# Kernel optimization log

Hardware: AMD Instinct MI355X
Metric: run time of the kernel (lower is better)

The kernel has to match this reference:

```python
import jax, jax.numpy as jnp
import numpy as np

B, T, HOR = 4096, 128, 24
EH, DH, A = 64, 64, 32


def setup_inputs() -> dict:
    key = jax.random.key(0)
    ks = jax.random.split(key, 21)
    g = lambda k, shape, s=0.1: (jax.random.normal(k, shape, jnp.float32) * s)
    return {
        "x": jax.random.normal(ks[0], (B, T, 1), jnp.float32),
        # encoder GRUCell (input_size=1)
        "W_ih_e": g(ks[1], (3 * EH, 1)), "W_hh_e": g(ks[2], (3 * EH, EH)),
        "b_ih_e": g(ks[3], (3 * EH,)), "b_hh_e": g(ks[4], (3 * EH,)),
        # encoder input attention
        "W_e": g(ks[5], (A, EH)), "U_e": g(ks[6], (1, A)),
        "b_e": jnp.zeros((1, A), jnp.float32), "v_e": g(ks[7], (A,)),
        # decoder init
        "W_init": g(ks[8], (DH, EH)), "b_init": g(ks[9], (DH,)),
        # decoder GRUCell (input_size=1)
        "W_ih_d": g(ks[10], (3 * DH, 1)), "W_hh_d": g(ks[11], (3 * DH, DH)),
        "b_ih_d": g(ks[12], (3 * DH,)), "b_hh_d": g(ks[13], (3 * DH,)),
        # temporal attention
        "W_d": g(ks[14], (A, DH)), "U_d": g(ks[15], (A, EH)), "v_d": g(ks[16], (A,)),
        # output head
        "W_out": g(ks[17], (1, DH + EH)), "b_out": g(ks[18], (1,)),
        "y0": jnp.zeros((1,), jnp.float32),
    }


def _gru_cell(x, h, W_ih, W_hh, b_ih, b_hh):
    # PyTorch GRUCell semantics
    gi = x @ W_ih.T + b_ih  # (B, 3H)
    gh = h @ W_hh.T + b_hh
    ir, iz, inn = jnp.split(gi, 3, axis=1)
    hr, hz, hn = jnp.split(gh, 3, axis=1)
    r = jax.nn.sigmoid(ir + hr)
    z = jax.nn.sigmoid(iz + hz)
    n = jnp.tanh(inn + r * hn)
    return (1.0 - z) * n + z * h


def reference(x, W_ih_e, W_hh_e, b_ih_e, b_hh_e, W_e, U_e, b_e, v_e,
              W_init, b_init, W_ih_d, W_hh_d, b_ih_d, b_hh_d,
              W_d, U_d, v_d, W_out, b_out, y0):
    bsz = x.shape[0]

    def enc_step(h, x_t):  # x_t: (B, 1)
        h_proj = h @ W_e.T  # (B, A)
        attn = jnp.tanh(h_proj[:, None, :] + x_t[:, :, None] * U_e[None] + b_e[None])  # (B,1,A)
        scores = jnp.sum(attn * v_e, axis=2)  # (B, 1)
        alpha = jax.nn.softmax(scores, axis=1)
        h_new = _gru_cell(alpha * x_t, h, W_ih_e, W_hh_e, b_ih_e, b_hh_e)
        return h_new, h_new

    h0 = jnp.zeros((bsz, EH), x.dtype)
    h_T, Hs = jax.lax.scan(enc_step, h0, jnp.swapaxes(x, 0, 1))  # Hs: (T,B,EH)
    H = jnp.swapaxes(Hs, 0, 1)  # (B, T, EH)

    d0 = h_T @ W_init.T + b_init  # (B, DH)
    H_proj = jnp.einsum('bte,ae->bta', H, U_d)  # hoisted: constant across decoder steps
    dec_in0 = jnp.broadcast_to(y0[None, :], (bsz, 1))

    def dec_step(carry, _):
        d, dec_in = carry
        d = _gru_cell(dec_in, d, W_ih_d, W_hh_d, b_ih_d, b_hh_d)
        d_proj = d @ W_d.T  # (B, A)
        attn = jnp.tanh(d_proj[:, None, :] + H_proj)  # (B, T, A)
        beta = jax.nn.softmax(jnp.sum(attn * v_d, axis=2), axis=1)  # (B, T)
        ctx = jnp.einsum('bt,bte->be', beta, H)  # (B, EH)
        out = jnp.concatenate([d, ctx], axis=1) @ W_out.T + b_out  # (B, 1)
        return (d, out), out[:, 0]

    (_, _), outs = jax.lax.scan(dec_step, (d0, dec_in0), None, length=HOR)
    return outs.T  # (B, horizon)
```

## Files before the change

kernel.cpp:

```cpp
#include <hip/hip_runtime.h>
#include <math.h>

#define BATCH 4096
#define T 128
#define HOR 24

#define LOG2E 1.44269504088896f
#define C2    2.88539008177793f

typedef _Float16 half2_t __attribute__((ext_vector_type(2)));
typedef _Float16 half8   __attribute__((ext_vector_type(8)));
typedef float f2  __attribute__((ext_vector_type(2)));
typedef float f4v __attribute__((ext_vector_type(4)));

__device__ __forceinline__ float fexp2(float x){ return __builtin_amdgcn_exp2f(x); }
__device__ __forceinline__ float frcp(float x){ return __builtin_amdgcn_rcpf(x); }
__device__ __forceinline__ float fsig(float x){ return frcp(1.0f + fexp2(-LOG2E*x)); }
__device__ __forceinline__ float ftanh(float x){ return fmaf(-2.0f, frcp(1.0f + fexp2(C2*x)), 1.0f); }
__device__ __forceinline__ half2_t bch(unsigned u){ return __builtin_bit_cast(half2_t,u); }
__device__ __forceinline__ unsigned pk2(float a,float b){ return __builtin_bit_cast(unsigned, __builtin_amdgcn_cvt_pkrtz(a,b)); }
__device__ __forceinline__ unsigned pk2rne(float a,float b){
  half2_t h; h.x = (_Float16)a; h.y = (_Float16)b;
  return __builtin_bit_cast(unsigned, h);
}
__device__ __forceinline__ float fdot2f(half2_t a, half2_t b, float c){
#if __has_builtin(__builtin_amdgcn_fdot2)
  return __builtin_amdgcn_fdot2(a,b,c,false);
#else
  return fmaf((float)a.x,(float)b.x, fmaf((float)a.y,(float)b.y,c));
#endif
}
__device__ __forceinline__ f2 pkfma(f2 a, f2 b, f2 c){ return __builtin_elementwise_fma(a,b,c); }

template <int CTRL, int RMASK>
__device__ __forceinline__ float dpp_add(float v) {
  int s = __builtin_amdgcn_update_dpp(0, __builtin_bit_cast(int, v), CTRL, RMASK, 0xf, true);
  return v + __builtin_bit_cast(float, s);
}
__device__ __forceinline__ float wavesum_dpp(float v) {
  v = dpp_add<0x111, 0xf>(v);
  v = dpp_add<0x112, 0xf>(v);
  v = dpp_add<0x114, 0xf>(v);
  v = dpp_add<0x118, 0xf>(v);
  v = dpp_add<0x142, 0xa>(v);
  v = dpp_add<0x143, 0xc>(v);
  return v;
}
__device__ __forceinline__ float rdl63(float v){
  return __builtin_bit_cast(float, __builtin_amdgcn_readlane(__builtin_bit_cast(int, v), 63));
}

#define WG_BARRIER_LDS() do {                                   \
    asm volatile("s_waitcnt lgkmcnt(0)" ::: "memory");          \
    __builtin_amdgcn_s_barrier();                               \
  } while (0)

__device__ __forceinline__ void gru_mv(const _Float16* hrow,
    const unsigned* wr_r, const unsigned* wr_z, const unsigned* wr_n,
    float& ar0, float& ar1, float& az0, float& az1, float& an0, float& an1)
{
  const uint4* hq = (const uint4*)hrow;
  #pragma unroll
  for (int q = 0; q < 8; ++q) {
    uint4 hv = hq[q];
    ar0 = fdot2f(bch(hv.x), bch(wr_r[4*q+0]), ar0);
    az0 = fdot2f(bch(hv.x), bch(wr_z[4*q+0]), az0);
    an0 = fdot2f(bch(hv.x), bch(wr_n[4*q+0]), an0);
    ar1 = fdot2f(bch(hv.y), bch(wr_r[4*q+1]), ar1);
    az1 = fdot2f(bch(hv.y), bch(wr_z[4*q+1]), az1);
    an1 = fdot2f(bch(hv.y), bch(wr_n[4*q+1]), an1);
    ar0 = fdot2f(bch(hv.z), bch(wr_r[4*q+2]), ar0);
    az0 = fdot2f(bch(hv.z), bch(wr_z[4*q+2]), az0);
    an0 = fdot2f(bch(hv.z), bch(wr_n[4*q+2]), an0);
    ar1 = fdot2f(bch(hv.w), bch(wr_r[4*q+3]), ar1);
    az1 = fdot2f(bch(hv.w), bch(wr_z[4*q+3]), az1);
    an1 = fdot2f(bch(hv.w), bch(wr_n[4*q+3]), an1);
  }
}

__device__ __forceinline__ float proj_dot(const _Float16* base, const unsigned* udr)
{
  float acc = 0.f;
  const uint4* hb = (const uint4*)base;
  #pragma unroll
  for (int q = 0; q < 4; ++q) {
    uint4 hv = hb[q];
    acc = fdot2f(bch(hv.x), bch(udr[4*q+0]), acc);
    acc = fdot2f(bch(hv.y), bch(udr[4*q+1]), acc);
    acc = fdot2f(bch(hv.z), bch(udr[4*q+2]), acc);
    acc = fdot2f(bch(hv.w), bch(udr[4*q+3]), acc);
  }
  return acc;
}

__device__ __forceinline__ half8 cvt8(f4v a, f4v b){
  half8 h;
  h[0]=(_Float16)a.x; h[1]=(_Float16)a.y; h[2]=(_Float16)a.z; h[3]=(_Float16)a.w;
  h[4]=(_Float16)b.x; h[5]=(_Float16)b.y; h[6]=(_Float16)b.z; h[7]=(_Float16)b.w;
  return h;
}

__device__ __forceinline__ float grp4(float acc, f4v ed,
                                      half2_t ha, half2_t hb,
                                      float v0, float v1, float v2, float v3)
{
  float a0 = fmaf(ed.x, (float)ha.x, 1.0f);
  float a1 = fmaf(ed.y, (float)ha.y, 1.0f);
  float a2 = fmaf(ed.z, (float)hb.x, 1.0f);
  float a3 = fmaf(ed.w, (float)hb.y, 1.0f);
  float d01 = a0 * a1;
  float d23 = a2 * a3;
  float n01 = fmaf(v0, a1, v1 * a0);
  float n23 = fmaf(v2, a3, v3 * a2);
  float nc  = fmaf(n01, d23, n23 * d01);
  return fmaf(nc, frcp(d01 * d23), acc);
}

__global__ __launch_bounds__(256, 1)
void darnn_enc(const float* __restrict__ x,
               const float* __restrict__ W_ih_e, const float* __restrict__ W_hh_e,
               const float* __restrict__ b_ih_e, const float* __restrict__ b_hh_e,
               const float* __restrict__ U_d, const float* __restrict__ W_out,
               unsigned* __restrict__ hpG, float* __restrict__ hTG)
{
  const int tid = threadIdx.x;
  const int w = tid >> 6;
  const int l = tid & 63;
  const int c = l & 15;
  const int q = l >> 4;
  const int e0 = blockIdx.x * 16;
  const int m0 = 16*w + 4*q;

  __shared__ __align__(16) _Float16 He[2][16*72];
  __shared__ __align__(16) unsigned xw[16*65];

  for (int idx = tid; idx < 16*64; idx += 256) {
    int e = idx >> 6, j = idx & 63;
    f2 g = ((const f2*)(x + (size_t)(e0+e)*T))[j];
    xw[e*65 + j] = pk2(g.x, g.y);
  }
  for (int idx = tid; idx < 576; idx += 256) ((unsigned*)He[0])[idx] = 0;

  half8 Ar[2], Az[2], An[2];
  #pragma unroll
  for (int kap = 0; kap < 2; ++kap) {
    const f4v* pr = (const f4v*)(W_hh_e + (size_t)(16*w + c)*64       + 32*kap + 8*q);
    const f4v* pz = (const f4v*)(W_hh_e + (size_t)(64 + 16*w + c)*64  + 32*kap + 8*q);
    const f4v* pn = (const f4v*)(W_hh_e + (size_t)(128 + 16*w + c)*64 + 32*kap + 8*q);
    Ar[kap] = cvt8(pr[0], pr[1]);
    Az[kap] = cvt8(pz[0], pz[1]);
    An[kap] = cvt8(pn[0], pn[1]);
  }
  half8 AX[2] = {{0,0,0,0,0,0,0,0},{0,0,0,0,0,0,0,0}};
  if (w < 2) {
    #pragma unroll
    for (int kap = 0; kap < 2; ++kap) {
      const f4v* p = (const f4v*)(U_d + (size_t)(16*w + c)*64 + 32*kap + 8*q);
      AX[kap] = cvt8(p[0] * C2, p[1] * C2);
    }
  } else if (w == 2 && c == 0) {
    #pragma unroll
    for (int kap = 0; kap < 2; ++kap) {
      const f4v* p = (const f4v*)(W_out + 64 + 32*kap + 8*q);
      AX[kap] = cvt8(p[0], p[1]);
    }
  }
  f4v wih0 = *(const f4v*)(W_ih_e + m0);
  f4v wih1 = *(const f4v*)(W_ih_e + 64 + m0);
  f4v wih2 = *(const f4v*)(W_ih_e + 128 + m0);
  f4v bb0  = *(const f4v*)(b_ih_e + m0)      + *(const f4v*)(b_hh_e + m0);
  f4v bb1  = *(const f4v*)(b_ih_e + 64 + m0) + *(const f4v*)(b_hh_e + 64 + m0);
  f4v bi2  = *(const f4v*)(b_ih_e + 128 + m0);
  f4v bh2  = *(const f4v*)(b_hh_e + 128 + m0);
  f4v hreg = {0,0,0,0};
  const f4v z4 = {0,0,0,0};
  unsigned* hpB = hpG + (size_t)(e0 + c) * 2176;

  __syncthreads();

  #pragma unroll 1
  for (int t = 0; t < T; ++t) {
    const _Float16* Hc = He[t & 1];
    half8 B0 = __builtin_bit_cast(half8, *(const uint4*)(Hc + c*72 + 8*q));
    half8 B1 = __builtin_bit_cast(half8, *(const uint4*)(Hc + c*72 + 32 + 8*q));
    if (t > 0) {
      if (w < 2) {
        f4v cu = __builtin_amdgcn_mfma_f32_16x16x32_f16(AX[0], B0, z4, 0,0,0);
        cu     = __builtin_amdgcn_mfma_f32_16x16x32_f16(AX[1], B1, cu, 0,0,0);
        unsigned* hpE = hpB + (t-1)*17 + 8*w;
        float x0 = fexp2(fminf(cu[0], 15.5f));
        float x1 = fexp2(fminf(cu[1], 15.5f));
        float x2 = fexp2(fminf(cu[2], 15.5f));
        float x3 = fexp2(fminf(cu[3], 15.5f));
        hpE[2*q]   = pk2rne(x0, x1);
        hpE[2*q+1] = pk2rne(x2, x3);
      } else if (w == 2) {
        f4v cw = __builtin_amdgcn_mfma_f32_16x16x32_f16(AX[0], B0, z4, 0,0,0);
        cw     = __builtin_amdgcn_mfma_f32_16x16x32_f16(AX[1], B1, cw, 0,0,0);
        if (q == 0) ((float*)(hpB + (t-1)*17))[16] = cw[0];
      }
    }
    f4v gr = __builtin_amdgcn_mfma_f32_16x16x32_f16(Ar[0], B0, z4, 0,0,0);
    gr     = __builtin_amdgcn_mfma_f32_16x16x32_f16(Ar[1], B1, gr, 0,0,0);
    f4v gz = __builtin_amdgcn_mfma_f32_16x16x32_f16(Az[0], B0, z4, 0,0,0);
    gz     = __builtin_amdgcn_mfma_f32_16x16x32_f16(Az[1], B1, gz, 0,0,0);
    f4v gn = __builtin_amdgcn_mfma_f32_16x16x32_f16(An[0], B0, z4, 0,0,0);
    gn     = __builtin_amdgcn_mfma_f32_16x16x32_f16(An[1], B1, gn, 0,0,0);
    float xc = (float)((const _Float16*)xw)[c*130 + t];
    f4v hn;
    #pragma unroll
    for (int i = 0; i < 4; ++i) {
      float r  = fsig(fmaf(xc, wih0[i], bb0[i]) + gr[i]);
      float zf = fsig(fmaf(xc, wih1[i], bb1[i]) + gz[i]);
      float n  = ftanh(fmaf(xc, wih2[i], bi2[i]) + r*(gn[i] + bh2[i]));
      float h  = fmaf(zf, hreg[i] - n, n);
      hreg[i] = h;
      hn[i] = h;
    }
    uint2 wv; wv.x = pk2(hn[0], hn[1]); wv.y = pk2(hn[2], hn[3]);
    *(uint2*)(He[(t+1)&1] + c*72 + m0) = wv;
    WG_BARRIER_LDS();
  }
  {
    const _Float16* Hc = He[0];
    half8 B0 = __builtin_bit_cast(half8, *(const uint4*)(Hc + c*72 + 8*q));
    half8 B1 = __builtin_bit_cast(half8, *(const uint4*)(Hc + c*72 + 32 + 8*q));
    if (w < 2) {
      f4v cu = __builtin_amdgcn_mfma_f32_16x16x32_f16(AX[0], B0, z4, 0,0,0);
      cu     = __builtin_amdgcn_mfma_f32_16x16x32_f16(AX[1], B1, cu, 0,0,0);
      unsigned* hpE = hpB + 127*17 + 8*w;
      float x0 = fexp2(fminf(cu[0], 15.5f));
      float x1 = fexp2(fminf(cu[1], 15.5f));
      float x2 = fexp2(fminf(cu[2], 15.5f));
      float x3 = fexp2(fminf(cu[3], 15.5f));
      hpE[2*q]   = pk2rne(x0, x1);
      hpE[2*q+1] = pk2rne(x2, x3);
    } else if (w == 2) {
      f4v cw = __builtin_amdgcn_mfma_f32_16x16x32_f16(AX[0], B0, z4, 0,0,0);
      cw     = __builtin_amdgcn_mfma_f32_16x16x32_f16(AX[1], B1, cw, 0,0,0);
      if (q == 0) ((float*)(hpB + 127*17))[16] = cw[0];
    }
  }
  #pragma unroll
  for (int i = 0; i < 4; ++i)
    hTG[(size_t)(e0 + c)*64 + m0 + i] = hreg[i];
}

__global__ __launch_bounds__(128, 2)
void darnn_dec(const float* __restrict__ W_init, const float* __restrict__ b_init,
               const float* __restrict__ W_ih_d, const float* __restrict__ W_hh_d,
               const float* __restrict__ b_ih_d, const float* __restrict__ b_hh_d,
               const float* __restrict__ W_d, const float* __restrict__ v_d,
               const float* __restrict__ W_out, const float* __restrict__ b_out,
               const float* __restrict__ y0,
               const unsigned* __restrict__ hpG, const float* __restrict__ hTG,
               float* __restrict__ out)
{
  const int tid = threadIdx.x;
  const int wid = tid >> 6;
  const int l   = tid & 63;
  const int bA  = 4*blockIdx.x + 2*wid;
  const int bB  = bA + 1;
  const int a    = l & 31;
  const int half = l >> 5;

  __shared__ __align__(16) unsigned char smem[36928];
  unsigned char* wbp = smem + wid*18464;
  unsigned* hpA   = (unsigned*)wbp;
  unsigned* hpB   = (unsigned*)(wbp + 8704);
  _Float16* ringA = (_Float16*)(wbp + 17408);
  _Float16* ringB = (_Float16*)(wbp + 17536);
  float*    dpA   = (float*)(wbp + 17664);
  float*    dpB   = (float*)(wbp + 17792);
  float*    hTA   = (float*)(wbp + 17920);
  float*    hTB   = (float*)(wbp + 18176);

  {
    const uint4* sA = (const uint4*)(hpG + (size_t)bA * 2176);
    const uint4* sB = (const uint4*)(hpG + (size_t)bB * 2176);
    #pragma unroll
    for (int it = 0; it < 8; ++it) {
      ((uint4*)hpA)[it*64 + l] = sA[it*64 + l];
      ((uint4*)hpB)[it*64 + l] = sB[it*64 + l];
    }
    const unsigned* rA = hpG + (size_t)bA*2176 + 2048;
    const unsigned* rB = hpG + (size_t)bB*2176 + 2048;
    hpA[2048 + l] = rA[l];      hpA[2112 + l] = rA[64 + l];
    hpB[2048 + l] = rB[l];      hpB[2112 + l] = rB[64 + l];
  }
  hTA[l] = hTG[(size_t)bA*64 + l];
  hTB[l] = hTG[(size_t)bB*64 + l];

  unsigned wr_r[32], wr_z[32], wr_n[32];
  {
    const f4v* wp = (const f4v*)W_hh_d;
    #pragma unroll
    for (int k = 0; k < 16; ++k) {
      f4v vr = wp[l*16 + k];
      f4v vz = wp[(64 + l)*16 + k];
      f4v vn = wp[(128 + l)*16 + k];
      wr_r[2*k] = pk2(vr.x, vr.y); wr_r[2*k+1] = pk2(vr.z, vr.w);
      wr_z[2*k] = pk2(vz.x, vz.y); wr_z[2*k+1] = pk2(vz.z, vz.w);
      wr_n[2*k] = pk2(vn.x, vn.y); wr_n[2*k+1] = pk2(vn.z, vn.w);
    }
  }
  float wih0 = W_ih_d[l], wih1 = W_ih_d[64+l], wih2 = W_ih_d[128+l];
  float bb0  = b_ih_d[l] + b_hh_d[l];
  float bb1  = b_ih_d[64+l] + b_hh_d[64+l];
  float bih2 = b_ih_d[128+l], bhh2 = b_hh_d[128+l];
  unsigned udr[16];
  {
    const f2* up = (const f2*)(W_d + a*64 + half*32);
    #pragma unroll
    for (int k = 0; k < 16; ++k) { f2 f = up[k]; udr[k] = pk2(f.x, f.y); }
  }
  float dprevA, dprevB;
  {
    const f4v* wi = (const f4v*)(W_init + l*64);
    const f4v* ga = (const f4v*)hTA;
    const f4v* gb = (const f4v*)hTB;
    f2 aa0={0,0}, aa1={0,0}, ba0={0,0}, ba1={0,0};
    #pragma unroll
    for (int k = 0; k < 16; ++k) {
      f4v wv = wi[k];
      f4v va = ga[k], vb = gb[k];
      aa0 = pkfma(wv.xy, va.xy, aa0);
      aa1 = pkfma(wv.zw, va.zw, aa1);
      ba0 = pkfma(wv.xy, vb.xy, ba0);
      ba1 = pkfma(wv.zw, vb.zw, ba1);
    }
    float bi = b_init[l];
    dprevA = bi + (aa0.x + aa0.y) + (aa1.x + aa1.y);
    dprevB = bi + (ba0.x + ba0.y) + (ba1.x + ba1.y);
  }
  float wout1 = W_out[l];
  float hw0A = __builtin_bit_cast(float, hpA[l*17 + 16]);
  float hw1A = __builtin_bit_cast(float, hpA[(64 + l)*17 + 16]);
  float hw0B = __builtin_bit_cast(float, hpB[l*17 + 16]);
  float hw1B = __builtin_bit_cast(float, hpB[(64 + l)*17 + 16]);
  float oprevA = y0[0], oprevB = y0[0];
  float bo = b_out[0];
  float c1;
  {
    float sv = v_d[a];
    sv += __shfl_xor(sv, 16); sv += __shfl_xor(sv, 8);
    sv += __shfl_xor(sv, 4);  sv += __shfl_xor(sv, 2); sv += __shfl_xor(sv, 1);
    c1 = LOG2E * sv;
  }
  ringA[l] = (_Float16)dprevA;
  ringB[l] = (_Float16)dprevB;

  const unsigned* hprA0 = hpA + l*17;
  const unsigned* hprA1 = hpA + (64 + l)*17;
  const unsigned* hprB0 = hpB + l*17;
  const unsigned* hprB1 = hpB + (64 + l)*17;

  #pragma unroll 1
  for (int s = 0; s < HOR; ++s) {
    float ar0A=0,ar1A=0,az0A=0,az1A=0,an0A=0,an1A=0;
    float ar0B=0,ar1B=0,az0B=0,az1B=0,an0B=0,an1B=0;
    gru_mv(ringA, wr_r, wr_z, wr_n, ar0A,ar1A,az0A,az1A,an0A,an1A);
    gru_mv(ringB, wr_r, wr_z, wr_n, ar0B,ar1B,az0B,az1B,an0B,an1B);
    float rA = fsig(fmaf(oprevA, wih0, bb0) + ar0A + ar1A);
    float zA = fsig(fmaf(oprevA, wih1, bb1) + az0A + az1A);
    float nA = ftanh(fmaf(oprevA, wih2, bih2) + rA * (an0A + an1A + bhh2));
    float dnewA = fmaf(zA, dprevA - nA, nA);
    float rB = fsig(fmaf(oprevB, wih0, bb0) + ar0B + ar1B);
    float zB = fsig(fmaf(oprevB, wih1, bb1) + az0B + az1B);
    float nB = ftanh(fmaf(oprevB, wih2, bih2) + rB * (an0B + an1B + bhh2));
    float dnewB = fmaf(zB, dprevB - nB, nB);
    dprevA = dnewA; dprevB = dnewB;
    ringA[l] = (_Float16)dnewA;
    ringB[l] = (_Float16)dnewB;
    {
      float accA = proj_dot(ringA + half*32, udr);
      float accB = proj_dot(ringB + half*32, udr);
      accA += __shfl_xor(accA, 32);
      accB += __shfl_xor(accB, 32);
      if (l < 32) {
        dpA[l] = fexp2(fminf(C2 * accA, 15.5f));
        dpB[l] = fexp2(fminf(C2 * accB, 15.5f));
      }
    }
    float rs0A = 0.f, rs1A = 0.f, rs0B = 0.f, rs1B = 0.f;
    #pragma unroll
    for (int j2 = 0; j2 < 8; ++j2) {
      f4v edA = *(const f4v*)&dpA[4*j2];
      f4v edB = *(const f4v*)&dpB[4*j2];
      half2_t haA0 = bch(hprA0[2*j2]), hbA0 = bch(hprA0[2*j2+1]);
      half2_t haA1 = bch(hprA1[2*j2]), hbA1 = bch(hprA1[2*j2+1]);
      half2_t haB0 = bch(hprB0[2*j2]), hbB0 = bch(hprB0[2*j2+1]);
      half2_t haB1 = bch(hprB1[2*j2]), hbB1 = bch(hprB1[2*j2+1]);
      float v0 = v_d[4*j2], v1 = v_d[4*j2+1], v2 = v_d[4*j2+2], v3 = v_d[4*j2+3];
      rs0A = grp4(rs0A, edA, haA0, hbA0, v0, v1, v2, v3);
      rs0B = grp4(rs0B, edB, haB0, hbB0, v0, v1, v2, v3);
      rs1A = grp4(rs1A, edA, haA1, hbA1, v0, v1, v2, v3);
      rs1B = grp4(rs1B, edB, haB1, hbB1, v0, v1, v2, v3);
    }
    float e0A = fexp2(fmaf(-C2, rs0A, c1));
    float e1A = fexp2(fmaf(-C2, rs1A, c1));
    float e0B = fexp2(fmaf(-C2, rs0B, c1));
    float e1B = fexp2(fmaf(-C2, rs1B, c1));
    float P0A = rdl63(wavesum_dpp(e0A + e1A));
    float P1A = rdl63(wavesum_dpp(fmaf(e0A, hw0A, e1A * hw1A)));
    float P2A = rdl63(wavesum_dpp(wout1 * dnewA));
    float P0B = rdl63(wavesum_dpp(e0B + e1B));
    float P1B = rdl63(wavesum_dpp(fmaf(e0B, hw0B, e1B * hw1B)));
    float P2B = rdl63(wavesum_dpp(wout1 * dnewB));
    float oA = fmaf(P1A, frcp(P0A), P2A + bo);
    float oB = fmaf(P1B, frcp(P0B), P2B + bo);
    if (l == 0) {
      out[(size_t)bA * HOR + s] = oA;
      out[(size_t)bB * HOR + s] = oB;
    }
    oprevA = oA; oprevB = oB;
  }
}

extern "C" void kernel_launch(void* const* d_in, const int* in_sizes, int n_in,
                              void* d_out, int out_size, void* d_ws, size_t ws_size,
                              hipStream_t stream) {
  const float* x      = (const float*)d_in[0];
  const float* W_ih_e = (const float*)d_in[1];
  const float* W_hh_e = (const float*)d_in[2];
  const float* b_ih_e = (const float*)d_in[3];
  const float* b_hh_e = (const float*)d_in[4];
  const float* W_init = (const float*)d_in[9];
  const float* b_init = (const float*)d_in[10];
  const float* W_ih_d = (const float*)d_in[11];
  const float* W_hh_d = (const float*)d_in[12];
  const float* b_ih_d = (const float*)d_in[13];
  const float* b_hh_d = (const float*)d_in[14];
  const float* W_d    = (const float*)d_in[15];
  const float* U_d    = (const float*)d_in[16];
  const float* v_d    = (const float*)d_in[17];
  const float* W_out  = (const float*)d_in[18];
  const float* b_out  = (const float*)d_in[19];
  const float* y0     = (const float*)d_in[20];
  float* outp = (float*)d_out;

  unsigned* hpG = (unsigned*)d_ws;
  float*    hTG = (float*)((char*)d_ws + (size_t)BATCH * 2176 * 4);

  darnn_enc<<<BATCH/16, 256, 0, stream>>>(x, W_ih_e, W_hh_e, b_ih_e, b_hh_e,
      U_d, W_out, hpG, hTG);
  darnn_dec<<<BATCH/4, 128, 0, stream>>>(W_init, b_init, W_ih_d, W_hh_d,
      b_ih_d, b_hh_d, W_d, v_d, W_out, b_out, y0, hpG, hTG, outp);
}
```

Before: 264.2 us.

## Split encoder GRU recurrence K-dimension across two wave groups with LDS reduction

The encoder block grows from 4 to 8 waves, and each pair of waves splits the 64-wide hidden K dimension of the recurrent matmul in half. Partial MFMA results are exchanged through LDS. The kp=0 waves then finish the GRU gate update while the kp=1 waves handle the attention-projection exp and output-weight work. The goal is to shorten the serial per-timestep critical path by halving MFMA chain length and moving side work off it. The cost is a second workgroup barrier per step plus extra LDS traffic, and the single He buffer adds a risk of read/write hazards.

```diff
diff --git a/kernel.cpp b/kernel.cpp
--- a/kernel.cpp
+++ b/kernel.cpp
@@ -116,7 +116,7 @@
   return fmaf(nc, frcp(d01 * d23), acc);
 }
 
-__global__ __launch_bounds__(256, 1)
+__global__ __launch_bounds__(512, 2)
 void darnn_enc(const float* __restrict__ x,
                const float* __restrict__ W_ih_e, const float* __restrict__ W_hh_e,
                const float* __restrict__ b_ih_e, const float* __restrict__ b_hh_e,
@@ -124,46 +124,44 @@
                unsigned* __restrict__ hpG, float* __restrict__ hTG)
 {
   const int tid = threadIdx.x;
-  const int w = tid >> 6;
-  const int l = tid & 63;
-  const int c = l & 15;
-  const int q = l >> 4;
-  const int e0 = blockIdx.x * 16;
-  const int m0 = 16*w + 4*q;
-
-  __shared__ __align__(16) _Float16 He[2][16*72];
+  const int w   = tid >> 6;
+  const int M   = w & 3;
+  const int kp  = w >> 2;
+  const int l   = tid & 63;
+  const int c   = l & 15;
+  const int q   = l >> 4;
+  const int e0  = blockIdx.x * 16;
+  const int m0  = 16*M + 4*q;
+
+  __shared__ __align__(16) _Float16 He[16*72];
   __shared__ __align__(16) unsigned xw[16*65];
-
-  for (int idx = tid; idx < 16*64; idx += 256) {
+  __shared__ __align__(16) uint4 Pg[4][3][64];
+  __shared__ __align__(16) uint4 Pe[3][64];
+
+  for (int idx = tid; idx < 16*64; idx += 512) {
     int e = idx >> 6, j = idx & 63;
     f2 g = ((const f2*)(x + (size_t)(e0+e)*T))[j];
     xw[e*65 + j] = pk2(g.x, g.y);
   }
-  for (int idx = tid; idx < 576; idx += 256) ((unsigned*)He[0])[idx] = 0;
-
-  half8 Ar[2], Az[2], An[2];
-  #pragma unroll
-  for (int kap = 0; kap < 2; ++kap) {
-    const f4v* pr = (const f4v*)(W_hh_e + (size_t)(16*w + c)*64       + 32*kap + 8*q);
-    const f4v* pz = (const f4v*)(W_hh_e + (size_t)(64 + 16*w + c)*64  + 32*kap + 8*q);
-    const f4v* pn = (const f4v*)(W_hh_e + (size_t)(128 + 16*w + c)*64 + 32*kap + 8*q);
-    Ar[kap] = cvt8(pr[0], pr[1]);
-    Az[kap] = cvt8(pz[0], pz[1]);
-    An[kap] = cvt8(pn[0], pn[1]);
-  }
-  half8 AX[2] = {{0,0,0,0,0,0,0,0},{0,0,0,0,0,0,0,0}};
-  if (w < 2) {
-    #pragma unroll
-    for (int kap = 0; kap < 2; ++kap) {
-      const f4v* p = (const f4v*)(U_d + (size_t)(16*w + c)*64 + 32*kap + 8*q);
-      AX[kap] = cvt8(p[0] * C2, p[1] * C2);
-    }
-  } else if (w == 2 && c == 0) {
-    #pragma unroll
-    for (int kap = 0; kap < 2; ++kap) {
-      const f4v* p = (const f4v*)(W_out + 64 + 32*kap + 8*q);
-      AX[kap] = cvt8(p[0], p[1]);
-    }
+  for (int idx = tid; idx < 576; idx += 512) ((unsigned*)He)[idx] = 0;
+
+  half8 Ar, Az, An;
+  {
+    const f4v* pr = (const f4v*)(W_hh_e + (size_t)(16*M + c)*64       + 32*kp + 8*q);
+    const f4v* pz = (const f4v*)(W_hh_e + (size_t)(64 + 16*M + c)*64  + 32*kp + 8*q);
+    const f4v* pn = (const f4v*)(W_hh_e + (size_t)(128 + 16*M + c)*64 + 32*kp + 8*q);
+    Ar = cvt8(pr[0], pr[1]);
+    Az = cvt8(pz[0], pz[1]);
+    An = cvt8(pn[0], pn[1]);
+  }
+  half8 AX = (half8){0,0,0,0,0,0,0,0};
+  half8 AW = (half8){0,0,0,0,0,0,0,0};
+  if (M < 2) {
+    const f4v* p = (const f4v*)(U_d + (size_t)(16*M + c)*64 + 32*kp + 8*q);
+    AX = cvt8(p[0] * C2, p[1] * C2);
+  } else if (M == 2 && c == 0) {
+    const f4v* p = (const f4v*)(W_out + 64 + 32*kp + 8*q);
+    AW = cvt8(p[0], p[1]);
   }
   f4v wih0 = *(const f4v*)(W_ih_e + m0);
   f4v wih1 = *(const f4v*)(W_ih_e + 64 + m0);
@@ -180,70 +178,87 @@
 
   #pragma unroll 1
   for (int t = 0; t < T; ++t) {
-    const _Float16* Hc = He[t & 1];
-    half8 B0 = __builtin_bit_cast(half8, *(const uint4*)(Hc + c*72 + 8*q));
-    half8 B1 = __builtin_bit_cast(half8, *(const uint4*)(Hc + c*72 + 32 + 8*q));
-    if (t > 0) {
-      if (w < 2) {
-        f4v cu = __builtin_amdgcn_mfma_f32_16x16x32_f16(AX[0], B0, z4, 0,0,0);
-        cu     = __builtin_amdgcn_mfma_f32_16x16x32_f16(AX[1], B1, cu, 0,0,0);
-        unsigned* hpE = hpB + (t-1)*17 + 8*w;
+    half8 B = __builtin_bit_cast(half8, *(const uint4*)(He + c*72 + 32*kp + 8*q));
+    f4v pgr = __builtin_amdgcn_mfma_f32_16x16x32_f16(Ar, B, z4, 0,0,0);
+    f4v pgz = __builtin_amdgcn_mfma_f32_16x16x32_f16(Az, B, z4, 0,0,0);
+    f4v pgn = __builtin_amdgcn_mfma_f32_16x16x32_f16(An, B, z4, 0,0,0);
+    f4v peh = z4, pw = z4;
+    if (M < 2)  peh = __builtin_amdgcn_mfma_f32_16x16x32_f16(AX, B, z4, 0,0,0);
+    if (M == 2) pw  = __builtin_amdgcn_mfma_f32_16x16x32_f16(AW, B, z4, 0,0,0);
+    if (kp == 1) {
+      Pg[M][0][l] = __builtin_bit_cast(uint4, pgr);
+      Pg[M][1][l] = __builtin_bit_cast(uint4, pgz);
+      Pg[M][2][l] = __builtin_bit_cast(uint4, pgn);
+    } else {
+      if (M < 2)  Pe[M][l] = __builtin_bit_cast(uint4, peh);
+      if (M == 2) Pe[2][l] = __builtin_bit_cast(uint4, pw);
+    }
+    WG_BARRIER_LDS();
+    if (kp == 0) {
+      f4v gr = pgr + __builtin_bit_cast(f4v, Pg[M][0][l]);
+      f4v gz = pgz + __builtin_bit_cast(f4v, Pg[M][1][l]);
+      f4v gn = pgn + __builtin_bit_cast(f4v, Pg[M][2][l]);
+      float xc = (float)((const _Float16*)xw)[c*130 + t];
+      f4v hn;
+      #pragma unroll
+      for (int i = 0; i < 4; ++i) {
+        float r  = fsig(fmaf(xc, wih0[i], bb0[i]) + gr[i]);
+        float zf = fsig(fmaf(xc, wih1[i], bb1[i]) + gz[i]);
+        float n  = ftanh(fmaf(xc, wih2[i], bi2[i]) + r*(gn[i] + bh2[i]));
+        float h  = fmaf(zf, hreg[i] - n, n);
+        hreg[i] = h;
+        hn[i] = h;
+      }
+      uint2 wv; wv.x = pk2(hn[0], hn[1]); wv.y = pk2(hn[2], hn[3]);
+      *(uint2*)(He + c*72 + m0) = wv;
+    } else if (t > 0) {
+      if (M < 2) {
+        f4v cu = peh + __builtin_bit_cast(f4v, Pe[M][l]);
+        unsigned* hpE = hpB + (t-1)*17 + 8*M;
         float x0 = fexp2(fminf(cu[0], 15.5f));
         float x1 = fexp2(fminf(cu[1], 15.5f));
         float x2 = fexp2(fminf(cu[2], 15.5f));
         float x3 = fexp2(fminf(cu[3], 15.5f));
         hpE[2*q]   = pk2rne(x0, x1);
         hpE[2*q+1] = pk2rne(x2, x3);
-      } else if (w == 2) {
-        f4v cw = __builtin_amdgcn_mfma_f32_16x16x32_f16(AX[0], B0, z4, 0,0,0);
-        cw     = __builtin_amdgcn_mfma_f32_16x16x32_f16(AX[1], B1, cw, 0,0,0);
+      } else if (M == 2) {
+        f4v cw = pw + __builtin_bit_cast(f4v, Pe[2][l]);
         if (q == 0) ((float*)(hpB + (t-1)*17))[16] = cw[0];
       }
     }
-    f4v gr = __builtin_amdgcn_mfma_f32_16x16x32_f16(Ar[0], B0, z4, 0,0,0);
-    gr     = __builtin_amdgcn_mfma_f32_16x16x32_f16(Ar[1], B1, gr, 0,0,0);
-    f4v gz = __builtin_amdgcn_mfma_f32_16x16x32_f16(Az[0], B0, z4, 0,0,0);
-    gz     = __builtin_amdgcn_mfma_f32_16x16x32_f16(Az[1], B1, gz, 0,0,0);
-    f4v gn = __builtin_amdgcn_mfma_f32_16x16x32_f16(An[0], B0, z4, 0,0,0);
-    gn     = __builtin_amdgcn_mfma_f32_16x16x32_f16(An[1], B1, gn, 0,0,0);
-    float xc = (float)((const _Float16*)xw)[c*130 + t];
-    f4v hn;
-    #pragma unroll
-    for (int i = 0; i < 4; ++i) {
-      float r  = fsig(fmaf(xc, wih0[i], bb0[i]) + gr[i]);
-      float zf = fsig(fmaf(xc, wih1[i], bb1[i]) + gz[i]);
-      float n  = ftanh(fmaf(xc, wih2[i], bi2[i]) + r*(gn[i] + bh2[i]));
-      float h  = fmaf(zf, hreg[i] - n, n);
-      hreg[i] = h;
-      hn[i] = h;
-    }
-    uint2 wv; wv.x = pk2(hn[0], hn[1]); wv.y = pk2(hn[2], hn[3]);
-    *(uint2*)(He[(t+1)&1] + c*72 + m0) = wv;
     WG_BARRIER_LDS();
   }
   {
-    const _Float16* Hc = He[0];
-    half8 B0 = __builtin_bit_cast(half8, *(const uint4*)(Hc + c*72 + 8*q));
-    half8 B1 = __builtin_bit_cast(half8, *(const uint4*)(Hc + c*72 + 32 + 8*q));
-    if (w < 2) {
-      f4v cu = __builtin_amdgcn_mfma_f32_16x16x32_f16(AX[0], B0, z4, 0,0,0);
-      cu     = __builtin_amdgcn_mfma_f32_16x16x32_f16(AX[1], B1, cu, 0,0,0);
-      unsigned* hpE = hpB + 127*17 + 8*w;
-      float x0 = fexp2(fminf(cu[0], 15.5f));
-      float x1 = fexp2(fminf(cu[1], 15.5f));
-      float x2 = fexp2(fminf(cu[2], 15.5f));
-      float x3 = fexp2(fminf(cu[3], 15.5f));
-      hpE[2*q]   = pk2rne(x0, x1);
-      hpE[2*q+1] = pk2rne(x2, x3);
-    } else if (w == 2) {
-      f4v cw = __builtin_amdgcn_mfma_f32_16x16x32_f16(AX[0], B0, z4, 0,0,0);
-      cw     = __builtin_amdgcn_mfma_f32_16x16x32_f16(AX[1], B1, cw, 0,0,0);
-      if (q == 0) ((float*)(hpB + 127*17))[16] = cw[0];
-    }
-  }
-  #pragma unroll
-  for (int i = 0; i < 4; ++i)
-    hTG[(size_t)(e0 + c)*64 + m0 + i] = hreg[i];
+    half8 B = __builtin_bit_cast(half8, *(const uint4*)(He + c*72 + 32*kp + 8*q));
+    f4v peh = z4, pw = z4;
+    if (M < 2)  peh = __builtin_amdgcn_mfma_f32_16x16x32_f16(AX, B, z4, 0,0,0);
+    if (M == 2) pw  = __builtin_amdgcn_mfma_f32_16x16x32_f16(AW, B, z4, 0,0,0);
+    if (kp == 0) {
+      if (M < 2)  Pe[M][l] = __builtin_bit_cast(uint4, peh);
+      if (M == 2) Pe[2][l] = __builtin_bit_cast(uint4, pw);
+    }
+    WG_BARRIER_LDS();
+    if (kp == 1) {
+      if (M < 2) {
+        f4v cu = peh + __builtin_bit_cast(f4v, Pe[M][l]);
+        unsigned* hpE = hpB + 127*17 + 8*M;
+        float x0 = fexp2(fminf(cu[0], 15.5f));
+        float x1 = fexp2(fminf(cu[1], 15.5f));
+        float x2 = fexp2(fminf(cu[2], 15.5f));
+        float x3 = fexp2(fminf(cu[3], 15.5f));
+        hpE[2*q]   = pk2rne(x0, x1);
+        hpE[2*q+1] = pk2rne(x2, x3);
+      } else if (M == 2) {
+        f4v cw = pw + __builtin_bit_cast(f4v, Pe[2][l]);
+        if (q == 0) ((float*)(hpB + 127*17))[16] = cw[0];
+      }
+    }
+  }
+  if (kp == 0) {
+    #pragma unroll
+    for (int i = 0; i < 4; ++i)
+      hTG[(size_t)(e0 + c)*64 + m0 + i] = hreg[i];
+  }
 }
 
 __global__ __launch_bounds__(128, 2)
@@ -442,7 +457,7 @@
   unsigned* hpG = (unsigned*)d_ws;
   float*    hTG = (float*)((char*)d_ws + (size_t)BATCH * 2176 * 4);
 
-  darnn_enc<<<BATCH/16, 256, 0, stream>>>(x, W_ih_e, W_hh_e, b_ih_e, b_hh_e,
+  darnn_enc<<<BATCH/16, 512, 0, stream>>>(x, W_ih_e, W_hh_e, b_ih_e, b_hh_e,
       U_d, W_out, hpG, hTG);
   darnn_dec<<<BATCH/4, 128, 0, stream>>>(W_init, b_init, W_ih_d, W_hh_d,
       b_ih_d, b_hh_d, W_d, v_d, W_out, b_out, y0, hpG, hTG, outp);
```

Result: slower. 282.3 us (+6.9%).

## Fuse encoder and decoder into one kernel keeping encoder outputs in LDS

Applied to the files above, without the earlier changes.

Merges the encoder and decoder into a single 512-thread kernel per 16-sequence block. The encoder runs on waves 0-3 and writes its per-timestep attention projections and final hidden state into shared memory instead of a global workspace. All eight waves then run the decoder, two sequences per wave, reading those values from LDS. This removes the global write and read of the large intermediate buffer and the second kernel launch. In exchange, the LDS footprint grows to nearly the full per-CU budget, which caps residency at one block per CU, and half the waves sit idle through the encoder loop.

```diff
diff --git a/kernel.cpp b/kernel.cpp
--- a/kernel.cpp
+++ b/kernel.cpp
@@ -116,119 +116,130 @@
   return fmaf(nc, frcp(d01 * d23), acc);
 }
 
-__global__ __launch_bounds__(256, 1)
-void darnn_enc(const float* __restrict__ x,
-               const float* __restrict__ W_ih_e, const float* __restrict__ W_hh_e,
-               const float* __restrict__ b_ih_e, const float* __restrict__ b_hh_e,
-               const float* __restrict__ U_d, const float* __restrict__ W_out,
-               unsigned* __restrict__ hpG, float* __restrict__ hTG)
+__global__ __launch_bounds__(512, 2)
+void darnn_fused(const float* __restrict__ x,
+                 const float* __restrict__ W_ih_e, const float* __restrict__ W_hh_e,
+                 const float* __restrict__ b_ih_e, const float* __restrict__ b_hh_e,
+                 const float* __restrict__ U_d, const float* __restrict__ W_out,
+                 const float* __restrict__ W_init, const float* __restrict__ b_init,
+                 const float* __restrict__ W_ih_d, const float* __restrict__ W_hh_d,
+                 const float* __restrict__ b_ih_d, const float* __restrict__ b_hh_d,
+                 const float* __restrict__ W_d, const float* __restrict__ v_d,
+                 const float* __restrict__ b_out, const float* __restrict__ y0,
+                 float* __restrict__ out)
 {
   const int tid = threadIdx.x;
-  const int w = tid >> 6;
-  const int l = tid & 63;
-  const int c = l & 15;
-  const int q = l >> 4;
-  const int e0 = blockIdx.x * 16;
-  const int m0 = 16*w + 4*q;
-
+  const int w   = tid >> 6;
+  const int l   = tid & 63;
+  const int c   = l & 15;
+  const int q   = l >> 4;
+  const int e0  = blockIdx.x * 16;
+
+  __shared__ __align__(16) unsigned EhS[16*2177];
   __shared__ __align__(16) _Float16 He[2][16*72];
   __shared__ __align__(16) unsigned xw[16*65];
-
-  for (int idx = tid; idx < 16*64; idx += 256) {
+  __shared__ __align__(16) float    hTS[16*64];
+  __shared__ __align__(16) unsigned decScr[8*128];
+
+  for (int idx = tid; idx < 16*64; idx += 512) {
     int e = idx >> 6, j = idx & 63;
     f2 g = ((const f2*)(x + (size_t)(e0+e)*T))[j];
     xw[e*65 + j] = pk2(g.x, g.y);
   }
-  for (int idx = tid; idx < 576; idx += 256) ((unsigned*)He[0])[idx] = 0;
-
+  for (int idx = tid; idx < 576; idx += 512) ((unsigned*)He[0])[idx] = 0;
+
+  const int mw = w & 3;
+  const int m0 = 16*mw + 4*q;
   half8 Ar[2], Az[2], An[2];
   #pragma unroll
   for (int kap = 0; kap < 2; ++kap) {
-    const f4v* pr = (const f4v*)(W_hh_e + (size_t)(16*w + c)*64       + 32*kap + 8*q);
-    const f4v* pz = (const f4v*)(W_hh_e + (size_t)(64 + 16*w + c)*64  + 32*kap + 8*q);
-    const f4v* pn = (const f4v*)(W_hh_e + (size_t)(128 + 16*w + c)*64 + 32*kap + 8*q);
+    const f4v* pr = (const f4v*)(W_hh_e + (size_t)(16*mw + c)*64       + 32*kap + 8*q);
+    const f4v* pz = (const f4v*)(W_hh_e + (size_t)(64 + 16*mw + c)*64  + 32*kap + 8*q);
+    const f4v* pn = (const f4v*)(W_hh_e + (size_t)(128 + 16*mw + c)*64 + 32*kap + 8*q);
     Ar[kap] = cvt8(pr[0], pr[1]);
     Az[kap] = cvt8(pz[0], pz[1]);
     An[kap] = cvt8(pn[0], pn[1]);
   }
   half8 AX[2] = {{0,0,0,0,0,0,0,0},{0,0,0,0,0,0,0,0}};
-  if (w < 2) {
+  if (mw < 2) {
     #pragma unroll
     for (int kap = 0; kap < 2; ++kap) {
-      const f4v* p = (const f4v*)(U_d + (size_t)(16*w + c)*64 + 32*kap + 8*q);
+      const f4v* p = (const f4v*)(U_d + (size_t)(16*mw + c)*64 + 32*kap + 8*q);
       AX[kap] = cvt8(p[0] * C2, p[1] * C2);
     }
-  } else if (w == 2 && c == 0) {
+  } else if (mw == 2 && c == 0) {
     #pragma unroll
     for (int kap = 0; kap < 2; ++kap) {
       const f4v* p = (const f4v*)(W_out + 64 + 32*kap + 8*q);
       AX[kap] = cvt8(p[0], p[1]);
     }
   }
-  f4v wih0 = *(const f4v*)(W_ih_e + m0);
-  f4v wih1 = *(const f4v*)(W_ih_e + 64 + m0);
-  f4v wih2 = *(const f4v*)(W_ih_e + 128 + m0);
-  f4v bb0  = *(const f4v*)(b_ih_e + m0)      + *(const f4v*)(b_hh_e + m0);
-  f4v bb1  = *(const f4v*)(b_ih_e + 64 + m0) + *(const f4v*)(b_hh_e + 64 + m0);
-  f4v bi2  = *(const f4v*)(b_ih_e + 128 + m0);
-  f4v bh2  = *(const f4v*)(b_hh_e + 128 + m0);
+  f4v wih0e = *(const f4v*)(W_ih_e + m0);
+  f4v wih1e = *(const f4v*)(W_ih_e + 64 + m0);
+  f4v wih2e = *(const f4v*)(W_ih_e + 128 + m0);
+  f4v bb0e  = *(const f4v*)(b_ih_e + m0)      + *(const f4v*)(b_hh_e + m0);
+  f4v bb1e  = *(const f4v*)(b_ih_e + 64 + m0) + *(const f4v*)(b_hh_e + 64 + m0);
+  f4v bi2e  = *(const f4v*)(b_ih_e + 128 + m0);
+  f4v bh2e  = *(const f4v*)(b_hh_e + 128 + m0);
   f4v hreg = {0,0,0,0};
   const f4v z4 = {0,0,0,0};
-  unsigned* hpB = hpG + (size_t)(e0 + c) * 2176;
+  unsigned* ehB = EhS + c*2177;
 
   __syncthreads();
 
   #pragma unroll 1
   for (int t = 0; t < T; ++t) {
-    const _Float16* Hc = He[t & 1];
-    half8 B0 = __builtin_bit_cast(half8, *(const uint4*)(Hc + c*72 + 8*q));
-    half8 B1 = __builtin_bit_cast(half8, *(const uint4*)(Hc + c*72 + 32 + 8*q));
-    if (t > 0) {
-      if (w < 2) {
-        f4v cu = __builtin_amdgcn_mfma_f32_16x16x32_f16(AX[0], B0, z4, 0,0,0);
-        cu     = __builtin_amdgcn_mfma_f32_16x16x32_f16(AX[1], B1, cu, 0,0,0);
-        unsigned* hpE = hpB + (t-1)*17 + 8*w;
-        float x0 = fexp2(fminf(cu[0], 15.5f));
-        float x1 = fexp2(fminf(cu[1], 15.5f));
-        float x2 = fexp2(fminf(cu[2], 15.5f));
-        float x3 = fexp2(fminf(cu[3], 15.5f));
-        hpE[2*q]   = pk2rne(x0, x1);
-        hpE[2*q+1] = pk2rne(x2, x3);
-      } else if (w == 2) {
-        f4v cw = __builtin_amdgcn_mfma_f32_16x16x32_f16(AX[0], B0, z4, 0,0,0);
-        cw     = __builtin_amdgcn_mfma_f32_16x16x32_f16(AX[1], B1, cw, 0,0,0);
-        if (q == 0) ((float*)(hpB + (t-1)*17))[16] = cw[0];
+    if (w < 4) {
+      const _Float16* Hc = He[t & 1];
+      half8 B0 = __builtin_bit_cast(half8, *(const uint4*)(Hc + c*72 + 8*q));
+      half8 B1 = __builtin_bit_cast(half8, *(const uint4*)(Hc + c*72 + 32 + 8*q));
+      if (t > 0) {
+        if (w < 2) {
+          f4v cu = __builtin_amdgcn_mfma_f32_16x16x32_f16(AX[0], B0, z4, 0,0,0);
+          cu     = __builtin_amdgcn_mfma_f32_16x16x32_f16(AX[1], B1, cu, 0,0,0);
+          unsigned* hpE = ehB + (t-1)*17 + 8*w;
+          float x0 = fexp2(fminf(cu[0], 15.5f));
+          float x1 = fexp2(fminf(cu[1], 15.5f));
+          float x2 = fexp2(fminf(cu[2], 15.5f));
+          float x3 = fexp2(fminf(cu[3], 15.5f));
+          hpE[2*q]   = pk2rne(x0, x1);
+          hpE[2*q+1] = pk2rne(x2, x3);
+        } else if (w == 2) {
+          f4v cw = __builtin_amdgcn_mfma_f32_16x16x32_f16(AX[0], B0, z4, 0,0,0);
+          cw     = __builtin_amdgcn_mfma_f32_16x16x32_f16(AX[1], B1, cw, 0,0,0);
+          if (q == 0) ((float*)(ehB + (t-1)*17))[16] = cw[0];
+        }
       }
-    }
-    f4v gr = __builtin_amdgcn_mfma_f32_16x16x32_f16(Ar[0], B0, z4, 0,0,0);
-    gr     = __builtin_amdgcn_mfma_f32_16x16x32_f16(Ar[1], B1, gr, 0,0,0);
-    f4v gz = __builtin_amdgcn_mfma_f32_16x16x32_f16(Az[0], B0, z4, 0,0,0);
-    gz     = __builtin_amdgcn_mfma_f32_16x16x32_f16(Az[1], B1, gz, 0,0,0);
-    f4v gn = __builtin_amdgcn_mfma_f32_16x16x32_f16(An[0], B0, z4, 0,0,0);
-    gn     = __builtin_amdgcn_mfma_f32_16x16x32_f16(An[1], B1, gn, 0,0,0);
-    float xc = (float)((const _Float16*)xw)[c*130 + t];
-    f4v hn;
-    #pragma unroll
-    for (int i = 0; i < 4; ++i) {
-      float r  = fsig(fmaf(xc, wih0[i], bb0[i]) + gr[i]);
-      float zf = fsig(fmaf(xc, wih1[i], bb1[i]) + gz[i]);
-      float n  = ftanh(fmaf(xc, wih2[i], bi2[i]) + r*(gn[i] + bh2[i]));
-      float h  = fmaf(zf, hreg[i] - n, n);
-      hreg[i] = h;
-      hn[i] = h;
-    }
-    uint2 wv; wv.x = pk2(hn[0], hn[1]); wv.y = pk2(hn[2], hn[3]);
-    *(uint2*)(He[(t+1)&1] + c*72 + m0) = wv;
+      f4v gr = __builtin_amdgcn_mfma_f32_16x16x32_f16(Ar[0], B0, z4, 0,0,0);
+      gr     = __builtin_amdgcn_mfma_f32_16x16x32_f16(Ar[1], B1, gr, 0,0,0);
+      f4v gz = __builtin_amdgcn_mfma_f32_16x16x32_f16(Az[0], B0, z4, 0,0,0);
+      gz     = __builtin_amdgcn_mfma_f32_16x16x32_f16(Az[1], B1, gz, 0,0,0);
+      f4v gn = __builtin_amdgcn_mfma_f32_16x16x32_f16(An[0], B0, z4, 0,0,0);
+      gn     = __builtin_amdgcn_mfma_f32_16x16x32_f16(An[1], B1, gn, 0,0,0);
+      float xc = (float)((const _Float16*)xw)[c*130 + t];
+      f4v hn;
+      #pragma unroll
+      for (int i = 0; i < 4; ++i) {
+        float r  = fsig(fmaf(xc, wih0e[i], bb0e[i]) + gr[i]);
+        float zf = fsig(fmaf(xc, wih1e[i], bb1e[i]) + gz[i]);
+        float n  = ftanh(fmaf(xc, wih2e[i], bi2e[i]) + r*(gn[i] + bh2e[i]));
+        float h  = fmaf(zf, hreg[i] - n, n);
+        hreg[i] = h;
+        hn[i] = h;
+      }
+      uint2 wv; wv.x = pk2(hn[0], hn[1]); wv.y = pk2(hn[2], hn[3]);
+      *(uint2*)(He[(t+1)&1] + c*72 + m0) = wv;
+    }
     WG_BARRIER_LDS();
   }
-  {
+  if (w < 4) {
     const _Float16* Hc = He[0];
     half8 B0 = __builtin_bit_cast(half8, *(const uint4*)(Hc + c*72 + 8*q));
     half8 B1 = __builtin_bit_cast(half8, *(const uint4*)(Hc + c*72 + 32 + 8*q));
     if (w < 2) {
       f4v cu = __builtin_amdgcn_mfma_f32_16x16x32_f16(AX[0], B0, z4, 0,0,0);
       cu     = __builtin_amdgcn_mfma_f32_16x16x32_f16(AX[1], B1, cu, 0,0,0);
-      unsigned* hpE = hpB + 127*17 + 8*w;
+      unsigned* hpE = ehB + 127*17 + 8*w;
       float x0 = fexp2(fminf(cu[0], 15.5f));
       float x1 = fexp2(fminf(cu[1], 15.5f));
       float x2 = fexp2(fminf(cu[2], 15.5f));
@@ -238,58 +249,28 @@
     } else if (w == 2) {
       f4v cw = __builtin_amdgcn_mfma_f32_16x16x32_f16(AX[0], B0, z4, 0,0,0);
       cw     = __builtin_amdgcn_mfma_f32_16x16x32_f16(AX[1], B1, cw, 0,0,0);
-      if (q == 0) ((float*)(hpB + 127*17))[16] = cw[0];
-    }
-  }
-  #pragma unroll
-  for (int i = 0; i < 4; ++i)
-    hTG[(size_t)(e0 + c)*64 + m0 + i] = hreg[i];
-}
-
-__global__ __launch_bounds__(128, 2)
-void darnn_dec(const float* __restrict__ W_init, const float* __restrict__ b_init,
-               const float* __restrict__ W_ih_d, const float* __restrict__ W_hh_d,
-               const float* __restrict__ b_ih_d, const float* __restrict__ b_hh_d,
-               const float* __restrict__ W_d, const float* __restrict__ v_d,
-               const float* __restrict__ W_out, const float* __restrict__ b_out,
-               const float* __restrict__ y0,
-               const unsigned* __restrict__ hpG, const float* __restrict__ hTG,
-               float* __restrict__ out)
-{
-  const int tid = threadIdx.x;
-  const int wid = tid >> 6;
-  const int l   = tid & 63;
-  const int bA  = 4*blockIdx.x + 2*wid;
-  const int bB  = bA + 1;
+      if (q == 0) ((float*)(ehB + 127*17))[16] = cw[0];
+    }
+    #pragma unroll
+    for (int i = 0; i < 4; ++i)
+      hTS[c*64 + m0 + i] = hreg[i];
+  }
+  WG_BARRIER_LDS();
+
+  const int eA = 2*w, eB = eA + 1;
   const int a    = l & 31;
   const int half = l >> 5;
-
-  __shared__ __align__(16) unsigned char smem[36928];
-  unsigned char* wbp = smem + wid*18464;
-  unsigned* hpA   = (unsigned*)wbp;
-  unsigned* hpB   = (unsigned*)(wbp + 8704);
-  _Float16* ringA = (_Float16*)(wbp + 17408);
-  _Float16* ringB = (_Float16*)(wbp + 17536);
-  float*    dpA   = (float*)(wbp + 17664);
-  float*    dpB   = (float*)(wbp + 17792);
-  float*    hTA   = (float*)(wbp + 17920);
-  float*    hTB   = (float*)(wbp + 18176);
-
-  {
-    const uint4* sA = (const uint4*)(hpG + (size_t)bA * 2176);
-    const uint4* sB = (const uint4*)(hpG + (size_t)bB * 2176);
-    #pragma unroll
-    for (int it = 0; it < 8; ++it) {
-      ((uint4*)hpA)[it*64 + l] = sA[it*64 + l];
-      ((uint4*)hpB)[it*64 + l] = sB[it*64 + l];
-    }
-    const unsigned* rA = hpG + (size_t)bA*2176 + 2048;
-    const unsigned* rB = hpG + (size_t)bB*2176 + 2048;
-    hpA[2048 + l] = rA[l];      hpA[2112 + l] = rA[64 + l];
-    hpB[2048 + l] = rB[l];      hpB[2112 + l] = rB[64 + l];
-  }
-  hTA[l] = hTG[(size_t)bA*64 + l];
-  hTB[l] = hTG[(size_t)bB*64 + l];
+  unsigned* wbase = decScr + w*128;
+  _Float16* ringA = (_Float16*)wbase;
+  _Float16* ringB = (_Float16*)(wbase + 32);
+  float*    dpA   = (float*)(wbase + 64);
+  float*    dpB   = (float*)(wbase + 96);
+  const float* hTA = hTS + eA*64;
+  const float* hTB = hTS + eB*64;
+  const unsigned* hprA0 = EhS + eA*2177 + l*17;
+  const unsigned* hprA1 = EhS + eA*2177 + (64+l)*17;
+  const unsigned* hprB0 = EhS + eB*2177 + l*17;
+  const unsigned* hprB1 = EhS + eB*2177 + (64+l)*17;
 
   unsigned wr_r[32], wr_z[32], wr_n[32];
   {
@@ -334,10 +315,10 @@
     dprevB = bi + (ba0.x + ba0.y) + (ba1.x + ba1.y);
   }
   float wout1 = W_out[l];
-  float hw0A = __builtin_bit_cast(float, hpA[l*17 + 16]);
-  float hw1A = __builtin_bit_cast(float, hpA[(64 + l)*17 + 16]);
-  float hw0B = __builtin_bit_cast(float, hpB[l*17 + 16]);
-  float hw1B = __builtin_bit_cast(float, hpB[(64 + l)*17 + 16]);
+  float hw0A = __builtin_bit_cast(float, hprA0[16]);
+  float hw1A = __builtin_bit_cast(float, hprA1[16]);
+  float hw0B = __builtin_bit_cast(float, hprB0[16]);
+  float hw1B = __builtin_bit_cast(float, hprB1[16]);
   float oprevA = y0[0], oprevB = y0[0];
   float bo = b_out[0];
   float c1;
@@ -349,11 +330,6 @@
   }
   ringA[l] = (_Float16)dprevA;
   ringB[l] = (_Float16)dprevB;
-
-  const unsigned* hprA0 = hpA + l*17;
-  const unsigned* hprA1 = hpA + (64 + l)*17;
-  const unsigned* hprB0 = hpB + l*17;
-  const unsigned* hprB1 = hpB + (64 + l)*17;
 
   #pragma unroll 1
   for (int s = 0; s < HOR; ++s) {
@@ -410,8 +386,8 @@
     float oA = fmaf(P1A, frcp(P0A), P2A + bo);
     float oB = fmaf(P1B, frcp(P0B), P2B + bo);
     if (l == 0) {
-      out[(size_t)bA * HOR + s] = oA;
-      out[(size_t)bB * HOR + s] = oB;
+      out[(size_t)(e0 + eA) * HOR + s] = oA;
+      out[(size_t)(e0 + eB) * HOR + s] = oB;
     }
     oprevA = oA; oprevB = oB;
   }
@@ -439,11 +415,7 @@
   const float* y0     = (const float*)d_in[20];
   float* outp = (float*)d_out;
 
-  unsigned* hpG = (unsigned*)d_ws;
-  float*    hTG = (float*)((char*)d_ws + (size_t)BATCH * 2176 * 4);
-
-  darnn_enc<<<BATCH/16, 256, 0, stream>>>(x, W_ih_e, W_hh_e, b_ih_e, b_hh_e,
-      U_d, W_out, hpG, hTG);
-  darnn_dec<<<BATCH/4, 128, 0, stream>>>(W_init, b_init, W_ih_d, W_hh_d,
-      b_ih_d, b_hh_d, W_d, v_d, W_out, b_out, y0, hpG, hTG, outp);
-}
+  darnn_fused<<<BATCH/16, 512, 0, stream>>>(x, W_ih_e, W_hh_e, b_ih_e, b_hh_e,
+      U_d, W_out, W_init, b_init, W_ih_d, W_hh_d, b_ih_d, b_hh_d,
+      W_d, v_d, b_out, y0, outp);
+}
```

After: 251.9 us. -4.6%, faster.
